# Optimization experiments

Hardware: AMD Instinct MI355X
Metric: run time of the kernel (lower is better)

Reference implementation:

```python
import jax, jax.numpy as jnp
import numpy as np

N = 8192
IN_C = 512
OUT_C = 256
ALPHA = 0.5  # leaky-relu negative slope used on attention scores
NEG_INF = jnp.float32(-9e15)


def setup_inputs() -> dict:
    key = jax.random.key(0)
    k_h, k_adj, k_W, k_a = jax.random.split(key, 4)
    h = jax.random.normal(k_h, (N, IN_C), dtype=jnp.float32)
    adj = jax.random.randint(k_adj, (N, N), 0, 2, dtype=jnp.int32)
    # xavier_uniform with gain=1.414
    gain = 1.414
    limW = gain * np.sqrt(6.0 / (IN_C + OUT_C))
    W = jax.random.uniform(k_W, (IN_C, OUT_C), dtype=jnp.float32, minval=-limW, maxval=limW)
    lima = gain * np.sqrt(6.0 / (2 * OUT_C + 1))
    a = jax.random.uniform(k_a, (2 * OUT_C, 1), dtype=jnp.float32, minval=-lima, maxval=lima)
    return {"h": h, "adj": adj, "W": W, "a": a}


def reference(h, adj, W, a):
    out_c = W.shape[1]
    Wh = h @ W                                   # [N, out]
    Wh1 = Wh @ a[:out_c]                         # [N, 1]
    Wh2 = Wh @ a[out_c:]                         # [N, 1]
    e = jax.nn.leaky_relu(Wh1 + Wh2.T, negative_slope=ALPHA)  # [N, N]
    scores = jnp.where(adj > 0, e, NEG_INF)
    attention = jax.nn.softmax(scores, axis=1)   # row-wise softmax
    h_prime = attention @ Wh                     # [N, out] weighted aggregation
    return jnp.maximum(h_prime, 0.0)             # concat=True -> relu
```

## Files before the change

### kernel.cpp

```cpp
#include <hip/hip_runtime.h>
#include <stdint.h>

#define GN  8192
#define GIC 512
#define GOC 256

typedef int   vint4   __attribute__((__vector_size__(16)));
typedef float vfloat4 __attribute__((__vector_size__(16)));

__device__ __forceinline__ float bf2f(uint16_t u) {
  union { uint32_t i; float f; } v; v.i = ((uint32_t)u) << 16; return v.f;
}
__device__ __forceinline__ uint16_t f2bf(float f) {
  union { uint32_t i; float f; } v; v.f = f;
  uint32_t lsb = (v.i >> 16) & 1u;
  v.i += 0x7fffu + lsb;
  return (uint16_t)(v.i >> 16);
}
__device__ __forceinline__ float lrelu(float x) { return x > 0.f ? x : 0.5f * x; }
__device__ __forceinline__ float ldin(const void* p, size_t idx, int isbf) {
  return isbf ? bf2f(((const uint16_t*)p)[idx]) : ((const float*)p)[idx];
}

__global__ __launch_bounds__(256) void k_fill(uint16_t* out, int n) {
  int i = blockIdx.x * 256 + threadIdx.x;
  if (i < n) out[i] = 0x40E0u;
}

__global__ void k_detect(const void* W, int* flag) {
  __shared__ float mx[64];
  int t = threadIdx.x;
  const uint16_t* p = (const uint16_t*)W;
  float m = 0.f;
  for (int k = 0; k < 4; ++k) {
    float v = fabsf(bf2f(p[t * 4 + k]));
    if (!(v <= 1.0f)) v = 1e30f;
    m = fmaxf(m, v);
  }
  mx[t] = m;
  __syncthreads();
  if (t == 0) {
    float mm = 0.f;
    for (int i = 0; i < 64; ++i) mm = fmaxf(mm, mx[i]);
    flag[0] = (mm < 0.5f) ? 1 : 0;
  }
}

__global__ __launch_bounds__(256) void k_wh(const void* __restrict__ h,
                                            const void* __restrict__ W,
                                            uint16_t* __restrict__ WhF,
                                            const int* __restrict__ flag) {
  const int isbf = flag[0];
  __shared__ float hs[8][GIC];
  const int t = threadIdx.x, i0 = blockIdx.x * 8;
  float acc[8] = {0.f, 0.f, 0.f, 0.f, 0.f, 0.f, 0.f, 0.f};
  const int c = t;
  if (isbf) {
    const uint16_t* hp = (const uint16_t*)h;
    const uint16_t* Wp = (const uint16_t*)W;
    for (int x = t; x < 512; x += 256) {
      int r = x >> 6, cc = (x & 63) * 8;
      int4 raw = *(const int4*)&hp[(size_t)(i0 + r) * GIC + cc];
      uint32_t u0 = (uint32_t)raw.x;
      uint32_t u1 = (uint32_t)raw.y;
      uint32_t u2 = (uint32_t)raw.z;
      uint32_t u3 = (uint32_t)raw.w;
      hs[r][cc + 0] = bf2f((uint16_t)(u0 & 0xffffu));
      hs[r][cc + 1] = bf2f((uint16_t)(u0 >> 16));
      hs[r][cc + 2] = bf2f((uint16_t)(u1 & 0xffffu));
      hs[r][cc + 3] = bf2f((uint16_t)(u1 >> 16));
      hs[r][cc + 4] = bf2f((uint16_t)(u2 & 0xffffu));
      hs[r][cc + 5] = bf2f((uint16_t)(u2 >> 16));
      hs[r][cc + 6] = bf2f((uint16_t)(u3 & 0xffffu));
      hs[r][cc + 7] = bf2f((uint16_t)(u3 >> 16));
    }
    __syncthreads();
    for (int k = 0; k < GIC; k += 4) {
      float w0 = bf2f(Wp[(size_t)(k + 0) * GOC + c]);
      float w1 = bf2f(Wp[(size_t)(k + 1) * GOC + c]);
      float w2 = bf2f(Wp[(size_t)(k + 2) * GOC + c]);
      float w3 = bf2f(Wp[(size_t)(k + 3) * GOC + c]);
#pragma unroll
      for (int r = 0; r < 8; ++r) {
        float4 hv = *(const float4*)&hs[r][k];
        acc[r] = fmaf(hv.x, w0, acc[r]);
        acc[r] = fmaf(hv.y, w1, acc[r]);
        acc[r] = fmaf(hv.z, w2, acc[r]);
        acc[r] = fmaf(hv.w, w3, acc[r]);
      }
    }
  } else {
    for (int x = t; x < 8 * GIC; x += 256) {
      int r = x >> 9, k = x & (GIC - 1);
      hs[r][k] = ldin(h, (size_t)(i0 + r) * GIC + k, 0);
    }
    __syncthreads();
    for (int k = 0; k < GIC; ++k) {
      float w = ldin(W, (size_t)k * GOC + c, 0);
#pragma unroll
      for (int r = 0; r < 8; ++r) acc[r] = fmaf(hs[r][k], w, acc[r]);
    }
  }
  int4 pk;
  pk.x = (int)((uint32_t)f2bf(acc[0]) | ((uint32_t)f2bf(acc[1]) << 16));
  pk.y = (int)((uint32_t)f2bf(acc[2]) | ((uint32_t)f2bf(acc[3]) << 16));
  pk.z = (int)((uint32_t)f2bf(acc[4]) | ((uint32_t)f2bf(acc[5]) << 16));
  pk.w = (int)((uint32_t)f2bf(acc[6]) | ((uint32_t)f2bf(acc[7]) << 16));
  *(int4*)&WhF[((size_t)blockIdx.x * GOC + c) * 8] = pk;
}

__global__ __launch_bounds__(256) void k_wha(const uint16_t* __restrict__ WhF,
                                             const void* __restrict__ a,
                                             float* __restrict__ Wh1,
                                             float* __restrict__ Wh2,
                                             const int* __restrict__ flag) {
  const int isbf = flag[0];
  __shared__ float s1[256], s2[256];
  const int i = blockIdx.x, c = threadIdx.x;
  float v = bf2f(WhF[((size_t)(i >> 3) * GOC + c) * 8 + (i & 7)]);
  s1[c] = v * ldin(a, c, isbf);
  s2[c] = v * ldin(a, GOC + c, isbf);
  __syncthreads();
  for (int o = 128; o > 0; o >>= 1) {
    if (c < o) { s1[c] += s1[c + o]; s2[c] += s2[c + o]; }
    __syncthreads();
  }
  if (c == 0) { Wh1[i] = s1[0]; Wh2[i] = s2[0]; }
}

__global__ __launch_bounds__(256) void k_w2max(const float* __restrict__ Wh2,
                                               float* __restrict__ w2m) {
  __shared__ float red[256];
  const int t = threadIdx.x;
  float m = -3e38f;
  for (int x = t; x < GN / 4; x += 256) {
    float4 v = ((const float4*)Wh2)[x];
    m = fmaxf(m, fmaxf(fmaxf(v.x, v.y), fmaxf(v.z, v.w)));
  }
  red[t] = m;
  __syncthreads();
  for (int o = 128; o > 0; o >>= 1) {
    if (t < o) red[t] = fmaxf(red[t], red[t + o]);
    __syncthreads();
  }
  if (t == 0) w2m[0] = red[0];
}

__global__ __launch_bounds__(256) void GraphAttentionLayer_P1_2834678415522_kernel(
    const int* __restrict__ adj, const uint16_t* __restrict__ WhF,
    const float* __restrict__ Wh1, const float* __restrict__ Wh2,
    const float* __restrict__ w2m, float* __restrict__ pO,
    float* __restrict__ pL) {
  __shared__ uint16_t pA[16][72];
  __shared__ float red16[16][16];
  __shared__ float sb1[16];
  __shared__ float sbM[16];
  const int t = threadIdx.x;
  const int rg = blockIdx.x >> 1;
  const int ch = blockIdx.x & 1;
  const int i0 = rg * 16;
  const int jb = ch * 4096;
  if (t < 16) {
    float b = Wh1[i0 + t];
    sb1[t] = b;
    sbM[t] = lrelu(b + w2m[0]);
  }
  __syncthreads();

  const int ar = t >> 4;
  const int c16 = t & 15;
  const int aj = c16 * 4;
  const float vb = sb1[ar];
  const float vM = sbM[ar];
  const int lane = t & 63, w = t >> 6;
  const int quad = lane >> 4, n16 = lane & 15;

  vfloat4 acc0 = {0.f, 0.f, 0.f, 0.f};
  vfloat4 acc1 = {0.f, 0.f, 0.f, 0.f};
  vfloat4 acc2 = {0.f, 0.f, 0.f, 0.f};
  vfloat4 acc3 = {0.f, 0.f, 0.f, 0.f};
  float lsum = 0.f;

  const size_t rowbase = (size_t)(i0 + ar) * GN + jb;
  int4   adjv = *(const int4*)&adj[rowbase + aj];
  float4 w2v  = *(const float4*)&Wh2[jb + aj];

  for (int jt = 0; jt < 4096; jt += 64) {
    float e0 = adjv.x > 0 ? lrelu(vb + w2v.x) : -9e15f;
    float e1 = adjv.y > 0 ? lrelu(vb + w2v.y) : -9e15f;
    float e2 = adjv.z > 0 ? lrelu(vb + w2v.z) : -9e15f;
    float e3 = adjv.w > 0 ? lrelu(vb + w2v.w) : -9e15f;
    float p0 = __expf(e0 - vM);
    float p1 = __expf(e1 - vM);
    float p2 = __expf(e2 - vM);
    float p3 = __expf(e3 - vM);
    uint32_t q0 = (uint32_t)f2bf(p0) | ((uint32_t)f2bf(p1) << 16);
    uint32_t q1 = (uint32_t)f2bf(p2) | ((uint32_t)f2bf(p3) << 16);
    *(uint32_t*)&pA[ar][aj]     = q0;
    *(uint32_t*)&pA[ar][aj + 2] = q1;
    lsum += (p0 + p1) + (p2 + p3);
    if (jt + 64 < 4096) {
      adjv = *(const int4*)&adj[rowbase + jt + 64 + aj];
      w2v  = *(const float4*)&Wh2[jb + jt + 64 + aj];
    }
    __syncthreads();
    vint4 a0 = *(const vint4*)&pA[n16][quad * 8];
    vint4 a1 = *(const vint4*)&pA[n16][32 + quad * 8];
    const int kb0 = ((jb + jt) >> 3) + quad;
    const uint16_t* bp0 = &WhF[((size_t)kb0 * GOC + w * 64 + n16) * 8];
    const uint16_t* bp1 = &WhF[((size_t)(kb0 + 4) * GOC + w * 64 + n16) * 8];
#pragma unroll
    for (int ct = 0; ct < 4; ++ct) {
      vint4 b0 = *(const vint4*)(bp0 + (size_t)ct * 16 * 8);
      vint4 b1 = *(const vint4*)(bp1 + (size_t)ct * 16 * 8);
      vfloat4* accp = ct == 0 ? &acc0 : ct == 1 ? &acc1 : ct == 2 ? &acc2 : &acc3;
      __asm__ volatile("s_nop 1\n\tv_mfma_f32_16x16x32_bf16 %0, %1, %2, %0"
                       : "+v"(*accp) : "v"(a0), "v"(b0));
      __asm__ volatile("s_nop 1\n\tv_mfma_f32_16x16x32_bf16 %0, %1, %2, %0"
                       : "+v"(*accp) : "v"(a1), "v"(b1));
    }
    __syncthreads();
  }

  red16[ar][c16] = lsum;
  __asm__ volatile("s_nop 7\n\ts_nop 7"
                   : "+v"(acc0), "+v"(acc1), "+v"(acc2), "+v"(acc3));
  __syncthreads();
  if (t < 16) {
    float s = 0.f;
    for (int i = 0; i < 16; ++i) s += red16[t][i];
    pL[(size_t)ch * GN + i0 + t] = s;
  }

#pragma unroll
  for (int ct = 0; ct < 4; ++ct) {
    const vfloat4 av = ct == 0 ? acc0 : ct == 1 ? acc1 : ct == 2 ? acc2 : acc3;
    const int col = w * 64 + ct * 16 + n16;
    pO[((size_t)ch * GN + i0 + quad * 4 + 0) * GOC + col] = av[0];
    pO[((size_t)ch * GN + i0 + quad * 4 + 1) * GOC + col] = av[1];
    pO[((size_t)ch * GN + i0 + quad * 4 + 2) * GOC + col] = av[2];
    pO[((size_t)ch * GN + i0 + quad * 4 + 3) * GOC + col] = av[3];
  }
}

__global__ __launch_bounds__(256) void k_comb(const float* __restrict__ pO,
                                              const float* __restrict__ pL,
                                              void* __restrict__ out,
                                              const int* __restrict__ flag) {
  const int isbf = flag[0];
  size_t gid = ((size_t)blockIdx.x * 256 + threadIdx.x) * 4;
  size_t row = gid >> 8;
  float4 a0 = *(const float4*)&pO[gid];
  float4 a1 = *(const float4*)&pO[(size_t)GN * GOC + gid];
  float il = 1.0f / (pL[row] + pL[GN + row]);
  float v0 = fmaxf((a0.x + a1.x) * il, 0.f);
  float v1 = fmaxf((a0.y + a1.y) * il, 0.f);
  float v2 = fmaxf((a0.z + a1.z) * il, 0.f);
  float v3 = fmaxf((a0.w + a1.w) * il, 0.f);
  if (isbf) {
    uint16_t* o = (uint16_t*)out;
    uint32_t q0 = (uint32_t)f2bf(v0) | ((uint32_t)f2bf(v1) << 16);
    uint32_t q1 = (uint32_t)f2bf(v2) | ((uint32_t)f2bf(v3) << 16);
    *(uint32_t*)&o[gid]     = q0;
    *(uint32_t*)&o[gid + 2] = q1;
  } else {
    float4 vv;
    vv.x = v0; vv.y = v1; vv.z = v2; vv.w = v3;
    *(float4*)&((float*)out)[gid] = vv;
  }
}

__global__ __launch_bounds__(256) void k_gat1(
    const int* __restrict__ adj, const uint16_t* __restrict__ WhF,
    const float* __restrict__ Wh1, const float* __restrict__ Wh2,
    const float* __restrict__ w2m, void* __restrict__ out,
    const int* __restrict__ flag) {
  const int isbf = flag[0];
  __shared__ uint16_t pA[16][72];
  __shared__ float red16[16][16];
  __shared__ float sb1[16];
  __shared__ float sbM[16];
  __shared__ float lcS[16];
  const int t = threadIdx.x;
  const int i0 = blockIdx.x * 16;
  if (t < 16) {
    float b = Wh1[i0 + t];
    sb1[t] = b;
    sbM[t] = lrelu(b + w2m[0]);
  }
  __syncthreads();

  const int ar = t >> 4;
  const int c16 = t & 15;
  const int aj = c16 * 4;
  const float vb = sb1[ar];
  const float vM = sbM[ar];
  const int lane = t & 63, w = t >> 6;
  const int quad = lane >> 4, n16 = lane & 15;

  vfloat4 acc0 = {0.f, 0.f, 0.f, 0.f};
  vfloat4 acc1 = {0.f, 0.f, 0.f, 0.f};
  vfloat4 acc2 = {0.f, 0.f, 0.f, 0.f};
  vfloat4 acc3 = {0.f, 0.f, 0.f, 0.f};
  float lsum = 0.f;

  const size_t rowbase = (size_t)(i0 + ar) * GN;
  int4   adjv = *(const int4*)&adj[rowbase + aj];
  float4 w2v  = *(const float4*)&Wh2[aj];

  for (int j0 = 0; j0 < GN; j0 += 64) {
    float e0 = adjv.x > 0 ? lrelu(vb + w2v.x) : -9e15f;
    float e1 = adjv.y > 0 ? lrelu(vb + w2v.y) : -9e15f;
    float e2 = adjv.z > 0 ? lrelu(vb + w2v.z) : -9e15f;
    float e3 = adjv.w > 0 ? lrelu(vb + w2v.w) : -9e15f;
    float p0 = __expf(e0 - vM);
    float p1 = __expf(e1 - vM);
    float p2 = __expf(e2 - vM);
    float p3 = __expf(e3 - vM);
    uint32_t q0 = (uint32_t)f2bf(p0) | ((uint32_t)f2bf(p1) << 16);
    uint32_t q1 = (uint32_t)f2bf(p2) | ((uint32_t)f2bf(p3) << 16);
    *(uint32_t*)&pA[ar][aj]     = q0;
    *(uint32_t*)&pA[ar][aj + 2] = q1;
    lsum += (p0 + p1) + (p2 + p3);
    if (j0 + 64 < GN) {
      adjv = *(const int4*)&adj[rowbase + j0 + 64 + aj];
      w2v  = *(const float4*)&Wh2[j0 + 64 + aj];
    }
    __syncthreads();
    vint4 a0 = *(const vint4*)&pA[n16][quad * 8];
    vint4 a1 = *(const vint4*)&pA[n16][32 + quad * 8];
    const int kb0 = (j0 >> 3) + quad;
    const uint16_t* bp0 = &WhF[((size_t)kb0 * GOC + w * 64 + n16) * 8];
    const uint16_t* bp1 = &WhF[((size_t)(kb0 + 4) * GOC + w * 64 + n16) * 8];
#pragma unroll
    for (int ct = 0; ct < 4; ++ct) {
      vint4 b0 = *(const vint4*)(bp0 + (size_t)ct * 16 * 8);
      vint4 b1 = *(const vint4*)(bp1 + (size_t)ct * 16 * 8);
      vfloat4* accp = ct == 0 ? &acc0 : ct == 1 ? &acc1 : ct == 2 ? &acc2 : &acc3;
      __asm__ volatile("s_nop 1\n\tv_mfma_f32_16x16x32_bf16 %0, %1, %2, %0"
                       : "+v"(*accp) : "v"(a0), "v"(b0));
      __asm__ volatile("s_nop 1\n\tv_mfma_f32_16x16x32_bf16 %0, %1, %2, %0"
                       : "+v"(*accp) : "v"(a1), "v"(b1));
    }
    __syncthreads();
  }

  red16[ar][c16] = lsum;
  __asm__ volatile("s_nop 7\n\ts_nop 7"
                   : "+v"(acc0), "+v"(acc1), "+v"(acc2), "+v"(acc3));
  __syncthreads();
  if (t < 16) {
    float s = 0.f;
    for (int i = 0; i < 16; ++i) s += red16[t][i];
    lcS[t] = 1.0f / s;
  }
  __syncthreads();

  const float il0 = lcS[quad * 4 + 0];
  const float il1 = lcS[quad * 4 + 1];
  const float il2 = lcS[quad * 4 + 2];
  const float il3 = lcS[quad * 4 + 3];
#pragma unroll
  for (int ct = 0; ct < 4; ++ct) {
    const vfloat4 av = ct == 0 ? acc0 : ct == 1 ? acc1 : ct == 2 ? acc2 : acc3;
    const int col = w * 64 + ct * 16 + n16;
    float v0 = fmaxf(av[0] * il0, 0.f);
    float v1 = fmaxf(av[1] * il1, 0.f);
    float v2 = fmaxf(av[2] * il2, 0.f);
    float v3 = fmaxf(av[3] * il3, 0.f);
    if (isbf) {
      uint16_t* o = (uint16_t*)out;
      o[(size_t)(i0 + quad * 4 + 0) * GOC + col] = f2bf(v0);
      o[(size_t)(i0 + quad * 4 + 1) * GOC + col] = f2bf(v1);
      o[(size_t)(i0 + quad * 4 + 2) * GOC + col] = f2bf(v2);
      o[(size_t)(i0 + quad * 4 + 3) * GOC + col] = f2bf(v3);
    } else {
      float* o = (float*)out;
      o[(size_t)(i0 + quad * 4 + 0) * GOC + col] = v0;
      o[(size_t)(i0 + quad * 4 + 1) * GOC + col] = v1;
      o[(size_t)(i0 + quad * 4 + 2) * GOC + col] = v2;
      o[(size_t)(i0 + quad * 4 + 3) * GOC + col] = v3;
    }
  }
}

extern "C" void kernel_launch(void* const* d_in, const int* in_sizes, int n_in,
                              void* d_out, int out_size, void* d_ws, size_t ws_size,
                              hipStream_t stream) {
  uint16_t* WhF = (uint16_t*)d_ws;
  float* Wh1  = (float*)(WhF + (size_t)GN * GOC);
  float* Wh2  = Wh1 + GN;
  float* pO   = Wh2 + GN;
  float* pL   = pO + (size_t)2 * GN * GOC;
  int*   flag = (int*)(pL + 2 * GN);
  float* w2m  = (float*)(flag + 1);
  size_t need = (size_t)((char*)(w2m + 1) - (char*)d_ws);
  const int use_split = (ws_size >= need) ? 1 : 0;

  const void* h = d_in[0]; const void* adj = d_in[1];
  const void* W = d_in[2]; const void* a = d_in[3];
  for (int i = 0; i < n_in; ++i) {
    long long s = in_sizes[i];
    if      (s == (long long)GN * GIC)  h   = d_in[i];
    else if (s == (long long)GN * GN)   adj = d_in[i];
    else if (s == (long long)GIC * GOC) W   = d_in[i];
    else if (s == 2LL * GOC)            a   = d_in[i];
  }
  if (!use_split) {
    flag = (int*)(Wh2 + GN);
    w2m  = (float*)(flag + 1);
  }

  const int n_out = GN * GOC;
  k_fill<<<(n_out + 255) / 256, 256, 0, stream>>>((uint16_t*)d_out, n_out);
  k_detect<<<1, 64, 0, stream>>>(W, flag);
  k_wh <<<GN / 8, 256, 0, stream>>>(h, W, WhF, flag);
  k_wha<<<GN, 256, 0, stream>>>(WhF, a, Wh1, Wh2, flag);
  k_w2max<<<1, 256, 0, stream>>>(Wh2, w2m);
  if (use_split) {
    GraphAttentionLayer_P1_2834678415522_kernel<<<GN / 8, 256, 0, stream>>>(
        (const int*)adj, WhF, Wh1, Wh2, w2m, pO, pL);
    k_comb<<<(GN * GOC) / 1024, 256, 0, stream>>>(pO, pL, d_out, flag);
  } else {
    k_gat1<<<GN / 16, 256, 0, stream>>>((const int*)adj, WhF, Wh1, Wh2, w2m,
                                        d_out, flag);
  }
}
```

Before: 519.9 us.

## Retile attention kernel to 32 rows x 4 column splits and fuse Wh projection

The attention-aggregation kernel now processes 32 rows per block over a quarter of the columns, issuing two MFMA row tiles per loaded Wh fragment to double B-operand reuse. The combine kernel sums four partial outputs and denominators. The separate per-row projection kernel for Wh1/Wh2 is folded into the Wh GEMM kernel using its fp32 accumulators, removing a launch and a reread of Wh. The change doubles the partial-output workspace and combine traffic, and it needs a larger workspace to take the split path.

```diff
diff --git a/kernel.cpp b/kernel.cpp
--- a/kernel.cpp
+++ b/kernel.cpp
@@ -48,7 +48,10 @@
 
 __global__ __launch_bounds__(256) void k_wh(const void* __restrict__ h,
                                             const void* __restrict__ W,
+                                            const void* __restrict__ a,
                                             uint16_t* __restrict__ WhF,
+                                            float* __restrict__ Wh1,
+                                            float* __restrict__ Wh2,
                                             const int* __restrict__ flag) {
   const int isbf = flag[0];
   __shared__ float hs[8][GIC];
@@ -107,25 +110,32 @@
   pk.z = (int)((uint32_t)f2bf(acc[4]) | ((uint32_t)f2bf(acc[5]) << 16));
   pk.w = (int)((uint32_t)f2bf(acc[6]) | ((uint32_t)f2bf(acc[7]) << 16));
   *(int4*)&WhF[((size_t)blockIdx.x * GOC + c) * 8] = pk;
-}
-
-__global__ __launch_bounds__(256) void k_wha(const uint16_t* __restrict__ WhF,
-                                             const void* __restrict__ a,
-                                             float* __restrict__ Wh1,
-                                             float* __restrict__ Wh2,
-                                             const int* __restrict__ flag) {
-  const int isbf = flag[0];
-  __shared__ float s1[256], s2[256];
-  const int i = blockIdx.x, c = threadIdx.x;
-  float v = bf2f(WhF[((size_t)(i >> 3) * GOC + c) * 8 + (i & 7)]);
-  s1[c] = v * ldin(a, c, isbf);
-  s2[c] = v * ldin(a, GOC + c, isbf);
+
+  const float a1c = ldin(a, c, isbf);
+  const float a2c = ldin(a, GOC + c, isbf);
+  __syncthreads();
+  float* s1 = &hs[0][0];
+  float* s2 = &hs[0][0] + 2048;
+#pragma unroll
+  for (int r = 0; r < 8; ++r) {
+    s1[r * 256 + c] = acc[r] * a1c;
+    s2[r * 256 + c] = acc[r] * a2c;
+  }
   __syncthreads();
   for (int o = 128; o > 0; o >>= 1) {
-    if (c < o) { s1[c] += s1[c + o]; s2[c] += s2[c + o]; }
-    __syncthreads();
-  }
-  if (c == 0) { Wh1[i] = s1[0]; Wh2[i] = s2[0]; }
+    if (c < o) {
+#pragma unroll
+      for (int r = 0; r < 8; ++r) {
+        s1[r * 256 + c] += s1[r * 256 + c + o];
+        s2[r * 256 + c] += s2[r * 256 + c + o];
+      }
+    }
+    __syncthreads();
+  }
+  if (t < 8) {
+    Wh1[i0 + t] = s1[t * 256];
+    Wh2[i0 + t] = s2[t * 256];
+  }
 }
 
 __global__ __launch_bounds__(256) void k_w2max(const float* __restrict__ Wh2,
@@ -151,61 +161,78 @@
     const float* __restrict__ Wh1, const float* __restrict__ Wh2,
     const float* __restrict__ w2m, float* __restrict__ pO,
     float* __restrict__ pL) {
-  __shared__ uint16_t pA[16][72];
-  __shared__ float red16[16][16];
-  __shared__ float sb1[16];
-  __shared__ float sbM[16];
+  __shared__ uint16_t pA[32][72];
+  __shared__ float red32[32][8];
+  __shared__ float sb1[32];
+  __shared__ float sbM[32];
   const int t = threadIdx.x;
-  const int rg = blockIdx.x >> 1;
-  const int ch = blockIdx.x & 1;
-  const int i0 = rg * 16;
-  const int jb = ch * 4096;
-  if (t < 16) {
+  const int rg = blockIdx.x >> 2;
+  const int ch = blockIdx.x & 3;
+  const int i0 = rg * 32;
+  const int jb = ch * 2048;
+  if (t < 32) {
     float b = Wh1[i0 + t];
     sb1[t] = b;
     sbM[t] = lrelu(b + w2m[0]);
   }
   __syncthreads();
 
-  const int ar = t >> 4;
-  const int c16 = t & 15;
-  const int aj = c16 * 4;
+  const int ar = t >> 3;
+  const int a8 = (t & 7) * 8;
   const float vb = sb1[ar];
   const float vM = sbM[ar];
   const int lane = t & 63, w = t >> 6;
   const int quad = lane >> 4, n16 = lane & 15;
 
-  vfloat4 acc0 = {0.f, 0.f, 0.f, 0.f};
-  vfloat4 acc1 = {0.f, 0.f, 0.f, 0.f};
-  vfloat4 acc2 = {0.f, 0.f, 0.f, 0.f};
-  vfloat4 acc3 = {0.f, 0.f, 0.f, 0.f};
+  vfloat4 aL0 = {0.f, 0.f, 0.f, 0.f};
+  vfloat4 aL1 = {0.f, 0.f, 0.f, 0.f};
+  vfloat4 aL2 = {0.f, 0.f, 0.f, 0.f};
+  vfloat4 aL3 = {0.f, 0.f, 0.f, 0.f};
+  vfloat4 aH0 = {0.f, 0.f, 0.f, 0.f};
+  vfloat4 aH1 = {0.f, 0.f, 0.f, 0.f};
+  vfloat4 aH2 = {0.f, 0.f, 0.f, 0.f};
+  vfloat4 aH3 = {0.f, 0.f, 0.f, 0.f};
   float lsum = 0.f;
 
   const size_t rowbase = (size_t)(i0 + ar) * GN + jb;
-  int4   adjv = *(const int4*)&adj[rowbase + aj];
-  float4 w2v  = *(const float4*)&Wh2[jb + aj];
-
-  for (int jt = 0; jt < 4096; jt += 64) {
-    float e0 = adjv.x > 0 ? lrelu(vb + w2v.x) : -9e15f;
-    float e1 = adjv.y > 0 ? lrelu(vb + w2v.y) : -9e15f;
-    float e2 = adjv.z > 0 ? lrelu(vb + w2v.z) : -9e15f;
-    float e3 = adjv.w > 0 ? lrelu(vb + w2v.w) : -9e15f;
+  int4   adjv0 = *(const int4*)&adj[rowbase + a8];
+  int4   adjv1 = *(const int4*)&adj[rowbase + a8 + 4];
+  float4 w2v0  = *(const float4*)&Wh2[jb + a8];
+  float4 w2v1  = *(const float4*)&Wh2[jb + a8 + 4];
+
+  for (int jt = 0; jt < 2048; jt += 64) {
+    float e0 = adjv0.x > 0 ? lrelu(vb + w2v0.x) : -9e15f;
+    float e1 = adjv0.y > 0 ? lrelu(vb + w2v0.y) : -9e15f;
+    float e2 = adjv0.z > 0 ? lrelu(vb + w2v0.z) : -9e15f;
+    float e3 = adjv0.w > 0 ? lrelu(vb + w2v0.w) : -9e15f;
+    float e4 = adjv1.x > 0 ? lrelu(vb + w2v1.x) : -9e15f;
+    float e5 = adjv1.y > 0 ? lrelu(vb + w2v1.y) : -9e15f;
+    float e6 = adjv1.z > 0 ? lrelu(vb + w2v1.z) : -9e15f;
+    float e7 = adjv1.w > 0 ? lrelu(vb + w2v1.w) : -9e15f;
     float p0 = __expf(e0 - vM);
     float p1 = __expf(e1 - vM);
     float p2 = __expf(e2 - vM);
     float p3 = __expf(e3 - vM);
-    uint32_t q0 = (uint32_t)f2bf(p0) | ((uint32_t)f2bf(p1) << 16);
-    uint32_t q1 = (uint32_t)f2bf(p2) | ((uint32_t)f2bf(p3) << 16);
-    *(uint32_t*)&pA[ar][aj]     = q0;
-    *(uint32_t*)&pA[ar][aj + 2] = q1;
-    lsum += (p0 + p1) + (p2 + p3);
-    if (jt + 64 < 4096) {
-      adjv = *(const int4*)&adj[rowbase + jt + 64 + aj];
-      w2v  = *(const float4*)&Wh2[jb + jt + 64 + aj];
-    }
-    __syncthreads();
-    vint4 a0 = *(const vint4*)&pA[n16][quad * 8];
-    vint4 a1 = *(const vint4*)&pA[n16][32 + quad * 8];
+    float p4 = __expf(e4 - vM);
+    float p5 = __expf(e5 - vM);
+    float p6 = __expf(e6 - vM);
+    float p7 = __expf(e7 - vM);
+    *(uint32_t*)&pA[ar][a8]     = (uint32_t)f2bf(p0) | ((uint32_t)f2bf(p1) << 16);
+    *(uint32_t*)&pA[ar][a8 + 2] = (uint32_t)f2bf(p2) | ((uint32_t)f2bf(p3) << 16);
+    *(uint32_t*)&pA[ar][a8 + 4] = (uint32_t)f2bf(p4) | ((uint32_t)f2bf(p5) << 16);
+    *(uint32_t*)&pA[ar][a8 + 6] = (uint32_t)f2bf(p6) | ((uint32_t)f2bf(p7) << 16);
+    lsum += ((p0 + p1) + (p2 + p3)) + ((p4 + p5) + (p6 + p7));
+    if (jt + 64 < 2048) {
+      adjv0 = *(const int4*)&adj[rowbase + jt + 64 + a8];
+      adjv1 = *(const int4*)&adj[rowbase + jt + 64 + a8 + 4];
+      w2v0  = *(const float4*)&Wh2[jb + jt + 64 + a8];
+      w2v1  = *(const float4*)&Wh2[jb + jt + 64 + a8 + 4];
+    }
+    __syncthreads();
+    vint4 xa0 = *(const vint4*)&pA[n16][quad * 8];
+    vint4 xa1 = *(const vint4*)&pA[n16][32 + quad * 8];
+    vint4 xb0 = *(const vint4*)&pA[16 + n16][quad * 8];
+    vint4 xb1 = *(const vint4*)&pA[16 + n16][32 + quad * 8];
     const int kb0 = ((jb + jt) >> 3) + quad;
     const uint16_t* bp0 = &WhF[((size_t)kb0 * GOC + w * 64 + n16) * 8];
     const uint16_t* bp1 = &WhF[((size_t)(kb0 + 4) * GOC + w * 64 + n16) * 8];
@@ -213,33 +240,46 @@
     for (int ct = 0; ct < 4; ++ct) {
       vint4 b0 = *(const vint4*)(bp0 + (size_t)ct * 16 * 8);
       vint4 b1 = *(const vint4*)(bp1 + (size_t)ct * 16 * 8);
-      vfloat4* accp = ct == 0 ? &acc0 : ct == 1 ? &acc1 : ct == 2 ? &acc2 : &acc3;
-      __asm__ volatile("s_nop 1\n\tv_mfma_f32_16x16x32_bf16 %0, %1, %2, %0"
-                       : "+v"(*accp) : "v"(a0), "v"(b0));
-      __asm__ volatile("s_nop 1\n\tv_mfma_f32_16x16x32_bf16 %0, %1, %2, %0"
-                       : "+v"(*accp) : "v"(a1), "v"(b1));
-    }
-    __syncthreads();
-  }
-
-  red16[ar][c16] = lsum;
+      vfloat4* pl = ct == 0 ? &aL0 : ct == 1 ? &aL1 : ct == 2 ? &aL2 : &aL3;
+      vfloat4* ph = ct == 0 ? &aH0 : ct == 1 ? &aH1 : ct == 2 ? &aH2 : &aH3;
+      __asm__ volatile("s_nop 1\n\tv_mfma_f32_16x16x32_bf16 %0, %1, %2, %0"
+                       : "+v"(*pl) : "v"(xa0), "v"(b0));
+      __asm__ volatile("s_nop 1\n\tv_mfma_f32_16x16x32_bf16 %0, %1, %2, %0"
+                       : "+v"(*pl) : "v"(xa1), "v"(b1));
+      __asm__ volatile("s_nop 1\n\tv_mfma_f32_16x16x32_bf16 %0, %1, %2, %0"
+                       : "+v"(*ph) : "v"(xb0), "v"(b0));
+      __asm__ volatile("s_nop 1\n\tv_mfma_f32_16x16x32_bf16 %0, %1, %2, %0"
+                       : "+v"(*ph) : "v"(xb1), "v"(b1));
+    }
+    __syncthreads();
+  }
+
+  red32[ar][t & 7] = lsum;
   __asm__ volatile("s_nop 7\n\ts_nop 7"
-                   : "+v"(acc0), "+v"(acc1), "+v"(acc2), "+v"(acc3));
-  __syncthreads();
-  if (t < 16) {
-    float s = 0.f;
-    for (int i = 0; i < 16; ++i) s += red16[t][i];
-    pL[(size_t)ch * GN + i0 + t] = s;
-  }
-
+                   : "+v"(aL0), "+v"(aL1), "+v"(aL2), "+v"(aL3),
+                     "+v"(aH0), "+v"(aH1), "+v"(aH2), "+v"(aH3));
+  __syncthreads();
+  if (t < 32) {
+    float4 v0 = *(const float4*)&red32[t][0];
+    float4 v1 = *(const float4*)&red32[t][4];
+    pL[(size_t)ch * GN + i0 + t] = ((v0.x + v0.y) + (v0.z + v0.w))
+                                 + ((v1.x + v1.y) + (v1.z + v1.w));
+  }
+
+  const size_t obase = (size_t)ch * GN + i0;
 #pragma unroll
   for (int ct = 0; ct < 4; ++ct) {
-    const vfloat4 av = ct == 0 ? acc0 : ct == 1 ? acc1 : ct == 2 ? acc2 : acc3;
+    const vfloat4 vL = ct == 0 ? aL0 : ct == 1 ? aL1 : ct == 2 ? aL2 : aL3;
+    const vfloat4 vH = ct == 0 ? aH0 : ct == 1 ? aH1 : ct == 2 ? aH2 : aH3;
     const int col = w * 64 + ct * 16 + n16;
-    pO[((size_t)ch * GN + i0 + quad * 4 + 0) * GOC + col] = av[0];
-    pO[((size_t)ch * GN + i0 + quad * 4 + 1) * GOC + col] = av[1];
-    pO[((size_t)ch * GN + i0 + quad * 4 + 2) * GOC + col] = av[2];
-    pO[((size_t)ch * GN + i0 + quad * 4 + 3) * GOC + col] = av[3];
+    pO[(obase + quad * 4 + 0) * GOC + col] = vL[0];
+    pO[(obase + quad * 4 + 1) * GOC + col] = vL[1];
+    pO[(obase + quad * 4 + 2) * GOC + col] = vL[2];
+    pO[(obase + quad * 4 + 3) * GOC + col] = vL[3];
+    pO[(obase + 16 + quad * 4 + 0) * GOC + col] = vH[0];
+    pO[(obase + 16 + quad * 4 + 1) * GOC + col] = vH[1];
+    pO[(obase + 16 + quad * 4 + 2) * GOC + col] = vH[2];
+    pO[(obase + 16 + quad * 4 + 3) * GOC + col] = vH[3];
   }
 }
 
@@ -252,17 +292,17 @@
   size_t row = gid >> 8;
   float4 a0 = *(const float4*)&pO[gid];
   float4 a1 = *(const float4*)&pO[(size_t)GN * GOC + gid];
-  float il = 1.0f / (pL[row] + pL[GN + row]);
-  float v0 = fmaxf((a0.x + a1.x) * il, 0.f);
-  float v1 = fmaxf((a0.y + a1.y) * il, 0.f);
-  float v2 = fmaxf((a0.z + a1.z) * il, 0.f);
-  float v3 = fmaxf((a0.w + a1.w) * il, 0.f);
+  float4 a2 = *(const float4*)&pO[(size_t)2 * GN * GOC + gid];
+  float4 a3 = *(const float4*)&pO[(size_t)3 * GN * GOC + gid];
+  float il = 1.0f / (pL[row] + pL[GN + row] + pL[2 * GN + row] + pL[3 * GN + row]);
+  float v0 = fmaxf((a0.x + a1.x + a2.x + a3.x) * il, 0.f);
+  float v1 = fmaxf((a0.y + a1.y + a2.y + a3.y) * il, 0.f);
+  float v2 = fmaxf((a0.z + a1.z + a2.z + a3.z) * il, 0.f);
+  float v3 = fmaxf((a0.w + a1.w + a2.w + a3.w) * il, 0.f);
   if (isbf) {
     uint16_t* o = (uint16_t*)out;
-    uint32_t q0 = (uint32_t)f2bf(v0) | ((uint32_t)f2bf(v1) << 16);
-    uint32_t q1 = (uint32_t)f2bf(v2) | ((uint32_t)f2bf(v3) << 16);
-    *(uint32_t*)&o[gid]     = q0;
-    *(uint32_t*)&o[gid + 2] = q1;
+    *(uint32_t*)&o[gid]     = (uint32_t)f2bf(v0) | ((uint32_t)f2bf(v1) << 16);
+    *(uint32_t*)&o[gid + 2] = (uint32_t)f2bf(v2) | ((uint32_t)f2bf(v3) << 16);
   } else {
     float4 vv;
     vv.x = v0; vv.y = v1; vv.z = v2; vv.w = v3;
@@ -317,10 +357,8 @@
     float p1 = __expf(e1 - vM);
     float p2 = __expf(e2 - vM);
     float p3 = __expf(e3 - vM);
-    uint32_t q0 = (uint32_t)f2bf(p0) | ((uint32_t)f2bf(p1) << 16);
-    uint32_t q1 = (uint32_t)f2bf(p2) | ((uint32_t)f2bf(p3) << 16);
-    *(uint32_t*)&pA[ar][aj]     = q0;
-    *(uint32_t*)&pA[ar][aj + 2] = q1;
+    *(uint32_t*)&pA[ar][aj]     = (uint32_t)f2bf(p0) | ((uint32_t)f2bf(p1) << 16);
+    *(uint32_t*)&pA[ar][aj + 2] = (uint32_t)f2bf(p2) | ((uint32_t)f2bf(p3) << 16);
     lsum += (p0 + p1) + (p2 + p3);
     if (j0 + 64 < GN) {
       adjv = *(const int4*)&adj[rowbase + j0 + 64 + aj];
@@ -391,11 +429,15 @@
   float* Wh1  = (float*)(WhF + (size_t)GN * GOC);
   float* Wh2  = Wh1 + GN;
   float* pO   = Wh2 + GN;
-  float* pL   = pO + (size_t)2 * GN * GOC;
-  int*   flag = (int*)(pL + 2 * GN);
+  float* pL   = pO + (size_t)4 * GN * GOC;
+  int*   flag = (int*)(pL + 4 * GN);
   float* w2m  = (float*)(flag + 1);
   size_t need = (size_t)((char*)(w2m + 1) - (char*)d_ws);
   const int use_split = (ws_size >= need) ? 1 : 0;
+  if (!use_split) {
+    flag = (int*)(Wh2 + GN);
+    w2m  = (float*)(flag + 1);
+  }
 
   const void* h = d_in[0]; const void* adj = d_in[1];
   const void* W = d_in[2]; const void* a = d_in[3];
@@ -406,19 +448,14 @@
     else if (s == (long long)GIC * GOC) W   = d_in[i];
     else if (s == 2LL * GOC)            a   = d_in[i];
   }
-  if (!use_split) {
-    flag = (int*)(Wh2 + GN);
-    w2m  = (float*)(flag + 1);
-  }
 
   const int n_out = GN * GOC;
   k_fill<<<(n_out + 255) / 256, 256, 0, stream>>>((uint16_t*)d_out, n_out);
   k_detect<<<1, 64, 0, stream>>>(W, flag);
-  k_wh <<<GN / 8, 256, 0, stream>>>(h, W, WhF, flag);
-  k_wha<<<GN, 256, 0, stream>>>(WhF, a, Wh1, Wh2, flag);
+  k_wh <<<GN / 8, 256, 0, stream>>>(h, W, a, WhF, Wh1, Wh2, flag);
   k_w2max<<<1, 256, 0, stream>>>(Wh2, w2m);
   if (use_split) {
-    GraphAttentionLayer_P1_2834678415522_kernel<<<GN / 8, 256, 0, stream>>>(
+    GraphAttentionLayer_P1_2834678415522_kernel<<<(GN / 32) * 4, 256, 0, stream>>>(
         (const int*)adj, WhF, Wh1, Wh2, w2m, pO, pL);
     k_comb<<<(GN * GOC) / 1024, 256, 0, stream>>>(pO, pL, d_out, flag);
   } else {
```

Measured after the change: 485.1 us (median of 2 runs). -6.7%, faster.
